# Optimization experiments

Measured on AMD Instinct MI355X. Metric: run time of the kernel, lower is better.

The kernel has to match this reference:

```python
import jax, jax.numpy as jnp
import numpy as np

BN_EPS = 1e-5
W_SCALE = 0.05  # keep pre-softmax logits in a sane range with random weights


def setup_inputs() -> dict:
    key = jax.random.key(0)
    ks = jax.random.split(key, 8)
    b, C, H, W = 2, 512, 80, 80
    Ck, Cv, Co = 256, 256, 512
    return {
        "x": jax.random.normal(ks[0], (b, C, H, W), dtype=jnp.float32),
        "wk": jax.random.normal(ks[1], (Ck, C), dtype=jnp.float32) * W_SCALE,
        "bk": jax.random.normal(ks[2], (Ck,), dtype=jnp.float32) * W_SCALE,
        "gamma": jnp.ones((Ck,), dtype=jnp.float32),
        "beta": jnp.zeros((Ck,), dtype=jnp.float32),
        "rmean": jnp.zeros((Ck,), dtype=jnp.float32),
        "rvar": jnp.ones((Ck,), dtype=jnp.float32),
        "wv": jax.random.normal(ks[3], (Cv, C), dtype=jnp.float32) * W_SCALE,
        "bv": jax.random.normal(ks[4], (Cv,), dtype=jnp.float32) * W_SCALE,
        "wW": jax.random.normal(ks[5], (Co, Cv), dtype=jnp.float32) * W_SCALE,
        "bW": jax.random.normal(ks[6], (Co,), dtype=jnp.float32) * W_SCALE,
    }


def reference(x, wk, bk, gamma, beta, rmean, rvar, wv, bv, wW, bW):
    b, C, H, Wd = x.shape
    N = H * Wd
    Ck = wk.shape[0]
    Cv = wv.shape[0]
    # f_key == f_query (shared module): 1x1 conv + BN(inference) + ReLU
    k = jnp.einsum('bchw,oc->bohw', x, wk) + bk[:, None, None]
    scale_bn = gamma / jnp.sqrt(rvar + BN_EPS)
    k = (k - rmean[:, None, None]) * scale_bn[:, None, None] + beta[:, None, None]
    k = jax.nn.relu(k).reshape(b, Ck, N)          # [b, Ck, N]
    q = jnp.transpose(k, (0, 2, 1))               # [b, N, Ck] (query shares weights with key)
    # f_value: plain 1x1 conv
    v = (jnp.einsum('bchw,oc->bohw', x, wv) + bv[:, None, None]).reshape(b, Cv, N)
    sim = jnp.einsum('bnc,bcm->bnm', q, k) * (Ck ** -0.5)  # [b, N, N]
    sim = jax.nn.softmax(sim, axis=-1)
    ctx = jnp.einsum('bnm,bvm->bvn', sim, v).reshape(b, Cv, H, Wd)
    out = jnp.einsum('bvhw,ov->bohw', ctx, wW) + bW[:, None, None]
    return out
```

## Files before the change

### kernel.cpp

```cpp
#include <hip/hip_runtime.h>
#include <stdint.h>

typedef __attribute__((ext_vector_type(8))) short bf16x8;
typedef __attribute__((ext_vector_type(4))) float f32x4;

__device__ __forceinline__ float bf2f(ushort u) {
    union { uint32_t i; float f; } v; v.i = ((uint32_t)u) << 16; return v.f;
}
__device__ __forceinline__ ushort f2bf(float f) {
    union { float f; uint32_t i; } v; v.f = f;
    uint32_t r = v.i + 0x7fff + ((v.i >> 16) & 1);
    return (ushort)(r >> 16);
}

typedef unsigned int uint_as1 __attribute__((address_space(1)));
typedef unsigned int uint_as3 __attribute__((address_space(3)));
__device__ __forceinline__ void async16(const void* g, void* l) {
    __builtin_amdgcn_global_load_lds((const uint_as1*)g, (uint_as3*)l, 16, 0, 0);
}


__global__ void cvt_f32_bf16(const float* __restrict__ in, ushort* __restrict__ out, int n) {
    int i = blockIdx.x * blockDim.x + threadIdx.x;
    if (i < n) out[i] = f2bf(in[i]);
}

__global__ void prep_bn(const float* __restrict__ bk, const float* __restrict__ gamma,
                        const float* __restrict__ beta, const float* __restrict__ rmean,
                        const float* __restrict__ rvar,
                        float* __restrict__ scaleA, float* __restrict__ shiftA) {
    int i = threadIdx.x;
    float s = gamma[i] * rsqrtf(rvar[i] + 1e-5f);
    scaleA[i] = 0.25f * s;
    shiftA[i] = 0.25f * ((bk[i] - rmean[i]) * s + beta[i]);
}

__global__ void transpose_cvt(const float* __restrict__ x, ushort* __restrict__ xt) {
    __shared__ float t[32][33];
    int b = blockIdx.z;
    int n0 = blockIdx.x * 32, c0 = blockIdx.y * 32;
    const float* xb = x + (size_t)b * 512 * 6400;
    ushort* xtb = xt + (size_t)b * 6400 * 512;
    int tx = threadIdx.x, ty = threadIdx.y;
    t[ty][tx] = xb[(size_t)(c0 + ty) * 6400 + n0 + tx];
    __syncthreads();
    xtb[(size_t)(n0 + ty) * 512 + c0 + tx] = f2bf(t[tx][ty]);
}

template <int EPI>
__global__ __launch_bounds__(256) void gemm_nt(
    const ushort* __restrict__ A, const ushort* __restrict__ B, void* __restrict__ Cout,
    int K, int lda, int ldb, int ldc,
    size_t zsa, size_t zsb, size_t zsc,
    const float* __restrict__ vec0, const float* __restrict__ vec1,
    float* __restrict__ rsum) {
    __shared__ __align__(16) ushort smem[6 * 4096];

    A += (size_t)blockIdx.z * zsa;
    B += (size_t)blockIdx.z * zsb;

    const int tid = threadIdx.x;
    const int lane = tid & 63, wave = tid >> 6;
    const int wm = wave & 1, wn = wave >> 1;
    const int bM = blockIdx.y * 128, bN = blockIdx.x * 128;

    const int sr = lane >> 2;
    const int sc = (lane & 3) * 8;
    const ushort* gA0 = A + (size_t)(bM + wave * 32 + sr) * lda + sc;
    const ushort* gA1 = gA0 + (size_t)16 * lda;
    const ushort* gB0 = B + (size_t)(bN + wave * 32 + sr) * ldb + sc;
    const ushort* gB1 = gB0 + (size_t)16 * ldb;
    ushort* lAw = &smem[wave * 1024];
    ushort* lBw = &smem[3 * 4096 + wave * 1024];

    const int rowA = wm * 64;
    const int rowB = wn * 64;
    const int fr = lane & 15;
    const int fk = (lane >> 4) * 8;

    f32x4 acc[4][4] = {};
    const int nT = K >> 5;

    auto stage = [&](int t, int buf) {
        const int k0 = t * 32;
        const int ob = buf * 4096;
        async16(gA0 + k0, lAw + ob);
        async16(gA1 + k0, lAw + ob + 512);
        async16(gB0 + k0, lBw + ob);
        async16(gB1 + k0, lBw + ob + 512);
    };

    stage(0, 0);
    if (nT > 1) stage(1, 1);

    for (int t = 0; t < nT; ++t) {
        if (t + 1 < nT) { asm volatile("s_waitcnt vmcnt(4)" ::: "memory"); }
        else            { asm volatile("s_waitcnt vmcnt(0)" ::: "memory"); }
        __builtin_amdgcn_sched_barrier(0);
        __builtin_amdgcn_s_barrier();
        __builtin_amdgcn_sched_barrier(0);
        if (t + 2 < nT) stage(t + 2, (t + 2) % 3);
        const int cur = t % 3;
        const ushort* lA = &smem[cur * 4096];
        const ushort* lB = &smem[3 * 4096 + cur * 4096];
        bf16x8 af[4], bff[4];
#pragma unroll
        for (int mi = 0; mi < 4; mi++)
            af[mi] = *(const bf16x8*)&lA[(rowA + mi * 16 + fr) * 32 + fk];
#pragma unroll
        for (int ni = 0; ni < 4; ni++)
            bff[ni] = *(const bf16x8*)&lB[(rowB + ni * 16 + fr) * 32 + fk];
#pragma unroll
        for (int mi = 0; mi < 4; mi++)
#pragma unroll
            for (int ni = 0; ni < 4; ni++)
                acc[mi][ni] = __builtin_amdgcn_mfma_f32_16x16x32_bf16(af[mi], bff[ni], acc[mi][ni], 0, 0, 0);
        __builtin_amdgcn_sched_barrier(0);
    }
    __builtin_amdgcn_s_barrier();
    __builtin_amdgcn_sched_barrier(0);

    float* Cf = (float*)Cout + (size_t)blockIdx.z * zsc;
    ushort* Cu = (ushort*)Cout + (size_t)blockIdx.z * zsc;
    float* lt = (float*)smem;
    const int g4 = (lane >> 4) * 4;
    const int cl = lane & 15;
    const int lr = tid >> 3;
    const int ch = tid & 7;

#pragma unroll
    for (int mi = 0; mi < 4; ++mi) {
#pragma unroll
        for (int ni = 0; ni < 4; ++ni) {
            const int lcol = wn * 64 + ni * 16 + cl;
#pragma unroll
            for (int r = 0; r < 4; ++r)
                lt[(wm * 16 + g4 + r) * 132 + lcol] = acc[mi][ni][r];
        }
        __syncthreads();
        {
            const int brow = (lr < 16) ? (mi * 16 + lr) : (64 + mi * 16 + (lr - 16));
            const int grow = bM + brow;
            const int gcol = bN + ch * 16;
            float vv[16];
#pragma unroll
            for (int i = 0; i < 16; i += 4) {
                f32x4 q = *(const f32x4*)&lt[lr * 132 + ch * 16 + i];
                vv[i] = q[0]; vv[i + 1] = q[1]; vv[i + 2] = q[2]; vv[i + 3] = q[3];
            }
            if (EPI == 1) {
#pragma unroll
                for (int i = 0; i < 16; i++)
                    vv[i] = fmaxf(vv[i] * vec0[gcol + i] + vec1[gcol + i], 0.f);
            }
            if (EPI == 2 || EPI == 3) {
                const float rb = vec0[grow];
#pragma unroll
                for (int i = 0; i < 16; i++) vv[i] += rb;
            }
            if (EPI == 5) {
                float ssum = 0.f;
#pragma unroll
                for (int i = 0; i < 16; i++) { vv[i] = __expf(vv[i]); ssum += vv[i]; }
                ssum += __shfl_down(ssum, 4, 8);
                ssum += __shfl_down(ssum, 2, 8);
                ssum += __shfl_down(ssum, 1, 8);
                if (ch == 0) rsum[(size_t)blockIdx.x * 6400 + grow] = ssum;
            }
            if (EPI == 3 || EPI == 4) {
#pragma unroll
                for (int i = 0; i < 16; i += 4) {
                    f32x4 q = { vv[i], vv[i + 1], vv[i + 2], vv[i + 3] };
                    *(f32x4*)&Cf[(size_t)grow * ldc + gcol + i] = q;
                }
            } else {
                ushort o16[16];
#pragma unroll
                for (int i = 0; i < 16; i++) o16[i] = f2bf(vv[i]);
                *(uint4*)&Cu[(size_t)grow * ldc + gcol] = *(const uint4*)&o16[0];
                *(uint4*)&Cu[(size_t)grow * ldc + gcol + 8] = *(const uint4*)&o16[8];
            }
        }
        __syncthreads();
    }
}

__global__ __launch_bounds__(256) void combine_inv(const float* __restrict__ rsum,
                                                   float* __restrict__ inv) {
    int r = blockIdx.x * 256 + threadIdx.x;
    float s = 0.f;
#pragma unroll
    for (int xb = 0; xb < 50; xb++) s += rsum[(size_t)xb * 6400 + r];
    inv[r] = 1.f / s;
}

__global__ __launch_bounds__(256) void reduce_ctx(const float* __restrict__ part, ushort* __restrict__ ctx,
                                                  const float* __restrict__ inv) {
    const size_t CH = 1638400;
    size_t i = ((size_t)blockIdx.x * 256 + threadIdx.x) * 4;
    float4 a = *(const float4*)&part[i];
#pragma unroll
    for (int c = 1; c < 5; c++) {
        float4 s = *(const float4*)&part[i + (size_t)c * CH];
        a.x += s.x; a.y += s.y; a.z += s.z; a.w += s.w;
    }
    const float w = inv[i >> 8];
    ushort o[4];
    o[0] = f2bf(a.x * w);
    o[1] = f2bf(a.y * w);
    o[2] = f2bf(a.z * w);
    o[3] = f2bf(a.w * w);
    *(uint2*)&ctx[i] = *(const uint2*)o;
}

extern "C" void kernel_launch(void* const* d_in, const int* in_sizes, int n_in,
                              void* d_out, int out_size, void* d_ws, size_t ws_size,
                              hipStream_t stream) {
    (void)in_sizes; (void)n_in; (void)out_size; (void)ws_size;
    const float* x     = (const float*)d_in[0];
    const float* wk    = (const float*)d_in[1];
    const float* bk    = (const float*)d_in[2];
    const float* gamma = (const float*)d_in[3];
    const float* beta  = (const float*)d_in[4];
    const float* rmean = (const float*)d_in[5];
    const float* rvar  = (const float*)d_in[6];
    const float* wv    = (const float*)d_in[7];
    const float* bv    = (const float*)d_in[8];
    const float* wW    = (const float*)d_in[9];
    const float* bW    = (const float*)d_in[10];
    float* out = (float*)d_out;

    ushort* Xt   = (ushort*)d_ws;
    ushort* wkb  = Xt + 6553600;
    ushort* wvb  = wkb + 131072;
    ushort* wWb  = wvb + 131072;
    ushort* Kt   = wWb + 131072;
    ushort* V    = Kt + 3276800;
    ushort* ctxT = V + 3276800;
    ushort* S    = ctxT + 3276800;
    float* scaleA = (float*)(S + 40960000);
    float* shiftA = scaleA + 256;
    float* rowsum = shiftA + 256;
    float* inv    = rowsum + 320000;
    float* part   = inv + 6400;

    cvt_f32_bf16<<<512, 256, 0, stream>>>(wk, wkb, 131072);
    cvt_f32_bf16<<<512, 256, 0, stream>>>(wv, wvb, 131072);
    cvt_f32_bf16<<<512, 256, 0, stream>>>(wW, wWb, 131072);
    prep_bn<<<1, 256, 0, stream>>>(bk, gamma, beta, rmean, rvar, scaleA, shiftA);
    transpose_cvt<<<dim3(200, 16, 2), dim3(32, 32), 0, stream>>>(x, Xt);

    gemm_nt<1><<<dim3(2, 50, 2), 256, 0, stream>>>(Xt, wkb, Kt, 512, 512, 512, 256,
                                                   3276800, 0, 1638400, scaleA, shiftA, nullptr);
    gemm_nt<2><<<dim3(50, 2, 2), 256, 0, stream>>>(wvb, Xt, V, 512, 512, 512, 6400,
                                                   0, 3276800, 1638400, bv, nullptr, nullptr);

    for (int b = 0; b < 2; b++) {
        ushort* Ktb  = Kt + (size_t)b * 1638400;
        ushort* Vb   = V  + (size_t)b * 1638400;
        ushort* ctxb = ctxT + (size_t)b * 1638400;
        gemm_nt<5><<<dim3(50, 50), 256, 0, stream>>>(Ktb, Ktb, S, 256, 256, 256, 6400,
                                                     0, 0, 0, nullptr, nullptr, rowsum);
        combine_inv<<<25, 256, 0, stream>>>(rowsum, inv);
        gemm_nt<4><<<dim3(2, 50, 5), 256, 0, stream>>>(S, Vb, part, 1280, 6400, 6400, 256,
                                                       1280, 1280, 1638400, nullptr, nullptr, nullptr);
        reduce_ctx<<<1600, 256, 0, stream>>>(part, ctxb, inv);
    }

    gemm_nt<3><<<dim3(50, 4, 2), 256, 0, stream>>>(wWb, ctxT, out, 256, 256, 256, 6400,
                                                   0, 1638400, 3276800, bW, nullptr, nullptr);
}
```

Before: 314.6 us.

## Add 128x256 wide-tile GEMM with LDS swizzle for attention GEMMs

Adds a gemm_wide kernel that uses 128x256 output tiles and XOR-swizzled LDS layout, and uses it for the similarity/exp GEMM and the S·V split-K GEMM. The split-K for S·V goes from 5 to 10 chunks, and the rowsum partial count and the reduce loops are adjusted to match. The float-to-bf16 conversion now uses the hardware v_cvt_pk_bf16_f32 instruction. The wider tiles are meant to raise operand reuse and cut LDS bank conflicts, at the cost of more accumulator registers and more partial-sum traffic in reduce_ctx.

```diff
diff --git a/kernel.cpp b/kernel.cpp
--- a/kernel.cpp
+++ b/kernel.cpp
@@ -4,13 +4,15 @@
 typedef __attribute__((ext_vector_type(8))) short bf16x8;
 typedef __attribute__((ext_vector_type(4))) float f32x4;
 
-__device__ __forceinline__ float bf2f(ushort u) {
-    union { uint32_t i; float f; } v; v.i = ((uint32_t)u) << 16; return v.f;
-}
 __device__ __forceinline__ ushort f2bf(float f) {
     union { float f; uint32_t i; } v; v.f = f;
     uint32_t r = v.i + 0x7fff + ((v.i >> 16) & 1);
     return (ushort)(r >> 16);
+}
+__device__ __forceinline__ uint32_t cvtpk(float lo, float hi) {
+    uint32_t r;
+    asm("v_cvt_pk_bf16_f32 %0, %1, %2" : "=v"(r) : "v"(lo), "v"(hi));
+    return r;
 }
 
 typedef unsigned int uint_as1 __attribute__((address_space(1)));
@@ -52,8 +54,7 @@
     const ushort* __restrict__ A, const ushort* __restrict__ B, void* __restrict__ Cout,
     int K, int lda, int ldb, int ldc,
     size_t zsa, size_t zsb, size_t zsc,
-    const float* __restrict__ vec0, const float* __restrict__ vec1,
-    float* __restrict__ rsum) {
+    const float* __restrict__ vec0, const float* __restrict__ vec1) {
     __shared__ __align__(16) ushort smem[6 * 4096];
 
     A += (size_t)blockIdx.z * zsa;
@@ -158,27 +159,163 @@
 #pragma unroll
                 for (int i = 0; i < 16; i++) vv[i] += rb;
             }
-            if (EPI == 5) {
-                float ssum = 0.f;
-#pragma unroll
-                for (int i = 0; i < 16; i++) { vv[i] = __expf(vv[i]); ssum += vv[i]; }
-                ssum += __shfl_down(ssum, 4, 8);
-                ssum += __shfl_down(ssum, 2, 8);
-                ssum += __shfl_down(ssum, 1, 8);
-                if (ch == 0) rsum[(size_t)blockIdx.x * 6400 + grow] = ssum;
-            }
-            if (EPI == 3 || EPI == 4) {
+            if (EPI == 3) {
 #pragma unroll
                 for (int i = 0; i < 16; i += 4) {
                     f32x4 q = { vv[i], vv[i + 1], vv[i + 2], vv[i + 3] };
                     *(f32x4*)&Cf[(size_t)grow * ldc + gcol + i] = q;
                 }
             } else {
-                ushort o16[16];
-#pragma unroll
-                for (int i = 0; i < 16; i++) o16[i] = f2bf(vv[i]);
-                *(uint4*)&Cu[(size_t)grow * ldc + gcol] = *(const uint4*)&o16[0];
-                *(uint4*)&Cu[(size_t)grow * ldc + gcol + 8] = *(const uint4*)&o16[8];
+                uint4 q0 = { cvtpk(vv[0], vv[1]), cvtpk(vv[2], vv[3]),
+                             cvtpk(vv[4], vv[5]), cvtpk(vv[6], vv[7]) };
+                uint4 q1 = { cvtpk(vv[8], vv[9]), cvtpk(vv[10], vv[11]),
+                             cvtpk(vv[12], vv[13]), cvtpk(vv[14], vv[15]) };
+                *(uint4*)&Cu[(size_t)grow * ldc + gcol] = q0;
+                *(uint4*)&Cu[(size_t)grow * ldc + gcol + 8] = q1;
+            }
+        }
+        __syncthreads();
+    }
+}
+
+template <int EPI>
+__global__ __launch_bounds__(256) void gemm_wide(
+    const ushort* __restrict__ A, const ushort* __restrict__ B, void* __restrict__ Cout,
+    int K, int lda, int ldb, int ldc,
+    size_t zsa, size_t zsb, size_t zsc,
+    float* __restrict__ rsum) {
+    __shared__ __align__(16) ushort smem[3 * 4096 + 3 * 8192];
+
+    A += (size_t)blockIdx.z * zsa;
+    B += (size_t)blockIdx.z * zsb;
+
+    const int tid = threadIdx.x;
+    const int lane = tid & 63, wave = tid >> 6;
+    const int wm = wave & 1, wn = wave >> 1;
+    const int bM = blockIdx.y * 128, bN = blockIdx.x * 256;
+
+    const int sr = lane >> 2;
+    const int scs = ((lane & 3) ^ ((lane >> 3) & 3)) * 8;
+    const ushort* gA0 = A + (size_t)(bM + wave * 32 + sr) * lda + scs;
+    const ushort* gA1 = gA0 + (size_t)16 * lda;
+    const ushort* gB0 = B + (size_t)(bN + wave * 64 + sr) * ldb + scs;
+    const ushort* gB1 = gB0 + (size_t)16 * ldb;
+    const ushort* gB2 = gB0 + (size_t)32 * ldb;
+    const ushort* gB3 = gB0 + (size_t)48 * ldb;
+    ushort* lAw = &smem[wave * 1024];
+    ushort* lBw = &smem[3 * 4096 + wave * 2048];
+
+    const int rowA = wm * 64;
+    const int rowB = wn * 128;
+    const int fr = lane & 15;
+    const int fq = lane >> 4;
+    const int fk = (fq ^ ((fr >> 1) & 3)) * 8;
+
+    f32x4 acc[4][8] = {};
+    const int nT = K >> 5;
+
+    auto stage = [&](int t, int buf) {
+        const int k0 = t * 32;
+        ushort* la = lAw + buf * 4096;
+        ushort* lb = lBw + buf * 8192;
+        async16(gA0 + k0, la);
+        async16(gA1 + k0, la + 512);
+        async16(gB0 + k0, lb);
+        async16(gB1 + k0, lb + 512);
+        async16(gB2 + k0, lb + 1024);
+        async16(gB3 + k0, lb + 1536);
+    };
+
+    stage(0, 0);
+    if (nT > 1) stage(1, 1);
+
+    for (int t = 0; t < nT; ++t) {
+        if (t + 1 < nT) { asm volatile("s_waitcnt vmcnt(6)" ::: "memory"); }
+        else            { asm volatile("s_waitcnt vmcnt(0)" ::: "memory"); }
+        __builtin_amdgcn_sched_barrier(0);
+        __builtin_amdgcn_s_barrier();
+        __builtin_amdgcn_sched_barrier(0);
+        if (t + 2 < nT) stage(t + 2, (t + 2) % 3);
+        const int cur = t % 3;
+        const ushort* lA = &smem[cur * 4096];
+        const ushort* lB = &smem[3 * 4096 + cur * 8192];
+        bf16x8 af[4], bff[8];
+#pragma unroll
+        for (int mi = 0; mi < 4; mi++)
+            af[mi] = *(const bf16x8*)&lA[(rowA + mi * 16 + fr) * 32 + fk];
+#pragma unroll
+        for (int ni = 0; ni < 8; ni++)
+            bff[ni] = *(const bf16x8*)&lB[(rowB + ni * 16 + fr) * 32 + fk];
+#pragma unroll
+        for (int mi = 0; mi < 4; mi++)
+#pragma unroll
+            for (int ni = 0; ni < 8; ni++)
+                acc[mi][ni] = __builtin_amdgcn_mfma_f32_16x16x32_bf16(af[mi], bff[ni], acc[mi][ni], 0, 0, 0);
+        __builtin_amdgcn_sched_barrier(0);
+    }
+    __builtin_amdgcn_s_barrier();
+    __builtin_amdgcn_sched_barrier(0);
+
+    float* Cf = (float*)Cout + (size_t)blockIdx.z * zsc;
+    ushort* Cu = (ushort*)Cout + (size_t)blockIdx.z * zsc;
+    float* lt = (float*)smem;
+    const int g4 = fq * 4;
+    const int cl = fr;
+    const int lr = tid >> 3;
+    const int ch = tid & 7;
+
+#pragma unroll
+    for (int mi = 0; mi < 4; ++mi) {
+#pragma unroll
+        for (int ni = 0; ni < 8; ++ni) {
+            const int lcol = wn * 128 + ni * 16 + cl;
+#pragma unroll
+            for (int r = 0; r < 4; ++r)
+                lt[(wm * 16 + g4 + r) * 260 + lcol] = acc[mi][ni][r];
+        }
+        __syncthreads();
+        {
+            const int brow = (lr < 16) ? (mi * 16 + lr) : (64 + mi * 16 + (lr - 16));
+            const int grow = bM + brow;
+            float vv[32];
+#pragma unroll
+            for (int h = 0; h < 2; ++h)
+#pragma unroll
+                for (int i = 0; i < 16; i += 4) {
+                    f32x4 q = *(const f32x4*)&lt[lr * 260 + h * 128 + ch * 16 + i];
+                    vv[h * 16 + i] = q[0]; vv[h * 16 + i + 1] = q[1];
+                    vv[h * 16 + i + 2] = q[2]; vv[h * 16 + i + 3] = q[3];
+                }
+            if (EPI == 5) {
+                float ssum = 0.f;
+#pragma unroll
+                for (int i = 0; i < 32; i++) { vv[i] = __expf(vv[i]); ssum += vv[i]; }
+                ssum += __shfl_down(ssum, 4, 8);
+                ssum += __shfl_down(ssum, 2, 8);
+                ssum += __shfl_down(ssum, 1, 8);
+                if (ch == 0) rsum[(size_t)blockIdx.x * 6400 + grow] = ssum;
+#pragma unroll
+                for (int h = 0; h < 2; ++h) {
+                    const int gcol = bN + h * 128 + ch * 16;
+                    const float* p = &vv[h * 16];
+                    uint4 q0 = { cvtpk(p[0], p[1]), cvtpk(p[2], p[3]),
+                                 cvtpk(p[4], p[5]), cvtpk(p[6], p[7]) };
+                    uint4 q1 = { cvtpk(p[8], p[9]), cvtpk(p[10], p[11]),
+                                 cvtpk(p[12], p[13]), cvtpk(p[14], p[15]) };
+                    *(uint4*)&Cu[(size_t)grow * ldc + gcol] = q0;
+                    *(uint4*)&Cu[(size_t)grow * ldc + gcol + 8] = q1;
+                }
+            } else {
+#pragma unroll
+                for (int h = 0; h < 2; ++h) {
+                    const int gcol = bN + h * 128 + ch * 16;
+#pragma unroll
+                    for (int i = 0; i < 16; i += 4) {
+                        f32x4 q = { vv[h * 16 + i], vv[h * 16 + i + 1],
+                                    vv[h * 16 + i + 2], vv[h * 16 + i + 3] };
+                        *(f32x4*)&Cf[(size_t)grow * ldc + gcol + i] = q;
+                    }
+                }
             }
         }
         __syncthreads();
@@ -190,7 +327,7 @@
     int r = blockIdx.x * 256 + threadIdx.x;
     float s = 0.f;
 #pragma unroll
-    for (int xb = 0; xb < 50; xb++) s += rsum[(size_t)xb * 6400 + r];
+    for (int xb = 0; xb < 25; xb++) s += rsum[(size_t)xb * 6400 + r];
     inv[r] = 1.f / s;
 }
 
@@ -200,17 +337,13 @@
     size_t i = ((size_t)blockIdx.x * 256 + threadIdx.x) * 4;
     float4 a = *(const float4*)&part[i];
 #pragma unroll
-    for (int c = 1; c < 5; c++) {
+    for (int c = 1; c < 10; c++) {
         float4 s = *(const float4*)&part[i + (size_t)c * CH];
         a.x += s.x; a.y += s.y; a.z += s.z; a.w += s.w;
     }
     const float w = inv[i >> 8];
-    ushort o[4];
-    o[0] = f2bf(a.x * w);
-    o[1] = f2bf(a.y * w);
-    o[2] = f2bf(a.z * w);
-    o[3] = f2bf(a.w * w);
-    *(uint2*)&ctx[i] = *(const uint2*)o;
+    uint2 o = { cvtpk(a.x * w, a.y * w), cvtpk(a.z * w, a.w * w) };
+    *(uint2*)&ctx[i] = o;
 }
 
 extern "C" void kernel_launch(void* const* d_in, const int* in_sizes, int n_in,
@@ -241,7 +374,7 @@
     float* scaleA = (float*)(S + 40960000);
     float* shiftA = scaleA + 256;
     float* rowsum = shiftA + 256;
-    float* inv    = rowsum + 320000;
+    float* inv    = rowsum + 160000;
     float* part   = inv + 6400;
 
     cvt_f32_bf16<<<512, 256, 0, stream>>>(wk, wkb, 131072);
@@ -251,22 +384,22 @@
     transpose_cvt<<<dim3(200, 16, 2), dim3(32, 32), 0, stream>>>(x, Xt);
 
     gemm_nt<1><<<dim3(2, 50, 2), 256, 0, stream>>>(Xt, wkb, Kt, 512, 512, 512, 256,
-                                                   3276800, 0, 1638400, scaleA, shiftA, nullptr);
+                                                   3276800, 0, 1638400, scaleA, shiftA);
     gemm_nt<2><<<dim3(50, 2, 2), 256, 0, stream>>>(wvb, Xt, V, 512, 512, 512, 6400,
-                                                   0, 3276800, 1638400, bv, nullptr, nullptr);
+                                                   0, 3276800, 1638400, bv, nullptr);
 
     for (int b = 0; b < 2; b++) {
         ushort* Ktb  = Kt + (size_t)b * 1638400;
         ushort* Vb   = V  + (size_t)b * 1638400;
         ushort* ctxb = ctxT + (size_t)b * 1638400;
-        gemm_nt<5><<<dim3(50, 50), 256, 0, stream>>>(Ktb, Ktb, S, 256, 256, 256, 6400,
-                                                     0, 0, 0, nullptr, nullptr, rowsum);
+        gemm_wide<5><<<dim3(25, 50), 256, 0, stream>>>(Ktb, Ktb, S, 256, 256, 256, 6400,
+                                                       0, 0, 0, rowsum);
         combine_inv<<<25, 256, 0, stream>>>(rowsum, inv);
-        gemm_nt<4><<<dim3(2, 50, 5), 256, 0, stream>>>(S, Vb, part, 1280, 6400, 6400, 256,
-                                                       1280, 1280, 1638400, nullptr, nullptr, nullptr);
+        gemm_wide<4><<<dim3(1, 50, 10), 256, 0, stream>>>(S, Vb, part, 640, 6400, 6400, 256,
+                                                          640, 640, 1638400, nullptr);
         reduce_ctx<<<1600, 256, 0, stream>>>(part, ctxb, inv);
     }
 
     gemm_nt<3><<<dim3(50, 4, 2), 256, 0, stream>>>(wWb, ctxT, out, 256, 256, 256, 6400,
-                                                   0, 1638400, 3276800, bW, nullptr, nullptr);
-}
+                                                   0, 1638400, 3276800, bW, nullptr);
+}
```

Result: slower. 338.1 us (+7.5%).
